# Kernel tuning notes

Measured on AMD Instinct MI355X. Metric: run time of the kernel, lower is better.

Reference implementation:

```python
import jax, jax.numpy as jnp
import numpy as np

NUM_CLUSTERS = 8
DIM_IN, DIM_HID = 1024, 256
N = 65536


def setup_inputs() -> dict:
    key = jax.random.key(0)
    ks = jax.random.split(key, 12)
    s_in = 1.0 / np.sqrt(DIM_IN)
    s_h = 1.0 / np.sqrt(DIM_HID)
    return {
        "x_path": jax.random.normal(ks[0], (1, N, DIM_IN), dtype=jnp.float32),
        "cluster_id": jax.random.randint(ks[1], (N,), 0, NUM_CLUSTERS),
        "W1": jax.random.normal(ks[2], (DIM_HID, DIM_IN), dtype=jnp.float32) * s_in,
        "b1": jax.random.normal(ks[3], (DIM_HID,), dtype=jnp.float32) * s_in,
        "Wf": jax.random.normal(ks[4], (DIM_HID, DIM_HID), dtype=jnp.float32) * s_h,
        "bf": jax.random.normal(ks[5], (DIM_HID,), dtype=jnp.float32) * s_h,
        "Wa": jax.random.normal(ks[6], (DIM_HID, DIM_HID), dtype=jnp.float32) * s_h,
        "ba": jax.random.normal(ks[7], (DIM_HID,), dtype=jnp.float32) * s_h,
        "Wb": jax.random.normal(ks[8], (DIM_HID, DIM_HID), dtype=jnp.float32) * s_h,
        "bb": jax.random.normal(ks[9], (DIM_HID,), dtype=jnp.float32) * s_h,
        "Wc": jax.random.normal(ks[10], (1, DIM_HID), dtype=jnp.float32) * s_h,
        "bc": jax.random.normal(ks[11], (1,), dtype=jnp.float32) * s_h,
    }


def reference(x_path, cluster_id, W1, b1, Wf, bf, Wa, ba, Wb, bb, Wc, bc):
    x = x_path[0]  # [N, dim_in]
    # per-instance 1x1 conv + ReLU (== linear + ReLU)
    h = jax.nn.relu(jnp.einsum('nd,hd->nh', x, W1) + b1)  # [N, dim_hid]
    # segment mean over clusters (AdaptiveAvgPool1d(1) per cluster); empty -> 0
    seg_sum = jax.ops.segment_sum(h, cluster_id, num_segments=NUM_CLUSTERS)
    counts = jax.ops.segment_sum(jnp.ones((h.shape[0],), h.dtype), cluster_id,
                                 num_segments=NUM_CLUSTERS)
    h_cluster = seg_sum / jnp.maximum(counts, 1.0)[:, None]  # [K, dim_hid]
    # attention net: Linear + ReLU (dropout is inference identity)
    h_path = jax.nn.relu(h_cluster @ Wf.T + bf)  # [K, dim_hid]
    # gated attention (CLAM Attn_Net_Gated)
    a = jnp.tanh(h_path @ Wa.T + ba)
    g = jax.nn.sigmoid(h_path @ Wb.T + bb)
    A = (a * g) @ Wc.T + bc            # [K, 1]
    A = jax.nn.softmax(A.T, axis=1)    # [1, K]
    H = A @ h_path                     # [1, dim_hid]
    return H
```

## Files before the change

kernel.cpp:

```cpp
#include <hip/hip_runtime.h>
#include <hip/hip_bf16.h>

#define NN    65536
#define KDIM  1024
#define HDIM  256
#define NC    8
#define BM    64
#define NPH   32

typedef __bf16 bf16x8 __attribute__((ext_vector_type(8)));
typedef float  f32x4  __attribute__((ext_vector_type(4)));
typedef __attribute__((address_space(1))) void GV;
typedef __attribute__((address_space(3))) void LV;

static __device__ __forceinline__ void async_cp16(const void* g, void* l) {
    __builtin_amdgcn_global_load_lds((GV*)g, (LV*)l, 16, 0, 0);
}

#define WAIT_VM6()        __builtin_amdgcn_s_waitcnt(0x0F76)
#define WAIT_VM4()        __builtin_amdgcn_s_waitcnt(0x0F74)
#define WAIT_VM6_LGKM0()  __builtin_amdgcn_s_waitcnt(0x0076)
#define SCHED_PIN()       __builtin_amdgcn_sched_barrier(0)

static __device__ __forceinline__ unsigned short f2bf_rne(float f) {
    unsigned int u = __float_as_uint(f);
    unsigned int r = u + 0x7fffu + ((u >> 16) & 1u);
    return (unsigned short)(r >> 16);
}

static __device__ __forceinline__ unsigned long long pack4bf(float4 v) {
    return (unsigned long long)f2bf_rne(v.x)
         | ((unsigned long long)f2bf_rne(v.y) << 16)
         | ((unsigned long long)f2bf_rne(v.z) << 32)
         | ((unsigned long long)f2bf_rne(v.w) << 48);
}

static __device__ __forceinline__ bf16x8 cvt8(f32x4 a, f32x4 b) {
    __hip_bfloat162 p0 = __float22bfloat162_rn(float2{a[0], a[1]});
    __hip_bfloat162 p1 = __float22bfloat162_rn(float2{a[2], a[3]});
    __hip_bfloat162 p2 = __float22bfloat162_rn(float2{b[0], b[1]});
    __hip_bfloat162 p3 = __float22bfloat162_rn(float2{b[2], b[3]});
    union { __hip_bfloat162 h[4]; bf16x8 v; } u;
    u.h[0] = p0; u.h[1] = p1; u.h[2] = p2; u.h[3] = p3;
    return u.v;
}

__global__ __launch_bounds__(256) void prep_kernel(
    const float* __restrict__ W1, unsigned short* __restrict__ W1b,
    const int* __restrict__ cid, int* __restrict__ cnt_partial)
{
    __shared__ int hcnt[NC];
    if (threadIdx.x < NC) hcnt[threadIdx.x] = 0;
    __syncthreads();

    const int gid  = blockIdx.x * 256 + threadIdx.x;
    const int lane = gid & 63;
    const int j    = (gid >> 6) & 3;
    const int wv   = (gid >> 8) & 3;
    const int kb   = gid >> 10;
    const int n    = wv * 64 + j * 16 + (lane & 15);
    const int k0   = kb * 32 + (lane >> 4) * 8;
    const float* src = W1 + (size_t)n * KDIM + k0;
    float4 v0 = *(const float4*)(src);
    float4 v1 = *(const float4*)(src + 4);
    ulonglong2 pk;
    pk.x = pack4bf(v0);
    pk.y = pack4bf(v1);
    *(ulonglong2*)(W1b + (size_t)gid * 8) = pk;

    atomicAdd(&hcnt[cid[gid]], 1);
    atomicAdd(&hcnt[cid[gid + 32768]], 1);
    __syncthreads();
    if (threadIdx.x < NC)
        cnt_partial[blockIdx.x * NC + threadIdx.x] = hcnt[threadIdx.x];
}

__global__ __launch_bounds__(256, 4) void gemm_kernel(
    const float* __restrict__ x, const int* __restrict__ cid,
    const unsigned short* __restrict__ W1b, const float* __restrict__ b1,
    float* __restrict__ partial)
{
    __shared__ __align__(16) char xs[3 * 8192];
    __shared__ float lsums[HDIM * NC];
    __shared__ int cids[BM];

    const int tid  = threadIdx.x;
    const int wave = tid >> 6;
    const int lane = tid & 63;
    const int l15  = lane & 15;
    const int q    = lane >> 4;
    const int row0 = blockIdx.x * BM;

    for (int i = tid; i < HDIM * NC; i += 256) lsums[i] = 0.0f;
    if (tid < BM) cids[tid] = cid[row0 + tid];

    const int rl = lane >> 3;
    const int cl = (lane & 7) ^ rl;
    const float* xg = x + (size_t)(row0 + wave * 16 + rl) * KDIM + cl * 4;

    const unsigned short* bg = W1b + (size_t)(wave * 256 + lane) * 8;

    const int le0 = l15 * 128 + (((2 * q + 0) ^ (l15 & 7)) * 16);
    const int le1 = l15 * 128 + (((2 * q + 1) ^ (l15 & 7)) * 16);

    f32x4 acc[4][4];
    #pragma unroll
    for (int i = 0; i < 4; ++i)
        #pragma unroll
        for (int j = 0; j < 4; ++j)
            #pragma unroll
            for (int r = 0; r < 4; ++r) acc[i][j][r] = 0.0f;

    bf16x8 bA[4], bB[4];

    #pragma unroll
    for (int h = 0; h < 2; ++h)
        async_cp16(xg + (size_t)h * 8 * KDIM, &xs[wave * 2048 + h * 1024]);
    #pragma unroll
    for (int j = 0; j < 4; ++j)
        bA[j] = *(const bf16x8*)(bg + j * 512);
    #pragma unroll
    for (int h = 0; h < 2; ++h)
        async_cp16(xg + (size_t)h * 8 * KDIM + 32, &xs[8192 + wave * 2048 + h * 1024]);
    SCHED_PIN();
    WAIT_VM6_LGKM0();
    __builtin_amdgcn_s_barrier();
    SCHED_PIN();

    #pragma unroll
    for (int kb = 0; kb < NPH; ++kb) {
        const int buf = kb % 3;
        bf16x8* curB = (kb & 1) ? bB : bA;
        bf16x8* nxtB = (kb & 1) ? bA : bB;

        if (kb + 1 < NPH) {
            #pragma unroll
            for (int j = 0; j < 4; ++j)
                nxtB[j] = *(const bf16x8*)(bg + (size_t)(kb + 1) * 8192 + j * 512);
        }
        if (kb + 2 < NPH) {
            const int b2 = (kb + 2) % 3;
            #pragma unroll
            for (int h = 0; h < 2; ++h)
                async_cp16(xg + (size_t)h * 8 * KDIM + (kb + 2) * 32,
                           &xs[b2 * 8192 + wave * 2048 + h * 1024]);
        }

        bf16x8 af[4];
        #pragma unroll
        for (int i = 0; i < 4; ++i) {
            const f32x4 v0 = *(const f32x4*)&xs[buf * 8192 + i * 2048 + le0];
            const f32x4 v1 = *(const f32x4*)&xs[buf * 8192 + i * 2048 + le1];
            af[i] = cvt8(v0, v1);
        }
        #pragma unroll
        for (int i = 0; i < 4; ++i)
            #pragma unroll
            for (int j = 0; j < 4; ++j)
                acc[i][j] = __builtin_amdgcn_mfma_f32_16x16x32_bf16(af[i], curB[j], acc[i][j], 0, 0, 0);

        if (kb < NPH - 2) {
            SCHED_PIN();
            if (kb < NPH - 2 - 1 + 1 && kb + 2 < NPH) WAIT_VM6(); else WAIT_VM4();
            __builtin_amdgcn_s_barrier();
            SCHED_PIN();
        } else if (kb == NPH - 2) {
            SCHED_PIN();
            WAIT_VM4();
            __builtin_amdgcn_s_barrier();
            SCHED_PIN();
        }
    }

    float b1v[4];
    #pragma unroll
    for (int j = 0; j < 4; ++j) b1v[j] = b1[wave * 64 + j * 16 + l15];

    #pragma unroll
    for (int i = 0; i < 4; ++i) {
        #pragma unroll
        for (int j = 0; j < 4; ++j) {
            const int col = wave * 64 + j * 16 + l15;
            #pragma unroll
            for (int r = 0; r < 4; ++r) {
                float v = fmaxf(acc[i][j][r] + b1v[j], 0.0f);
                int m = i * 16 + q * 4 + r;
                atomicAdd(&lsums[col * NC + cids[m]], v);
            }
        }
    }
    __syncthreads();
    float* dst = partial + (size_t)blockIdx.x * 2048 + tid * 8;
    *(f32x4*)dst       = *(const f32x4*)&lsums[tid * 8];
    *(f32x4*)(dst + 4) = *(const f32x4*)&lsums[tid * 8 + 4];
}

__global__ __launch_bounds__(256) void reduce_kernel(
    const float* __restrict__ partial, float* __restrict__ stage2)
{
    const int s  = blockIdx.x >> 3;
    const int og = blockIdx.x & 7;
    const int o  = og * 256 + threadIdx.x;
    const float* p = partial + (size_t)s * 128 * 2048 + o;
    float a0=0,a1=0,a2=0,a3=0,a4=0,a5=0,a6=0,a7=0;
    #pragma unroll 4
    for (int pb = 0; pb < 128; pb += 8) {
        a0 += p[(size_t)(pb+0)*2048]; a1 += p[(size_t)(pb+1)*2048];
        a2 += p[(size_t)(pb+2)*2048]; a3 += p[(size_t)(pb+3)*2048];
        a4 += p[(size_t)(pb+4)*2048]; a5 += p[(size_t)(pb+5)*2048];
        a6 += p[(size_t)(pb+6)*2048]; a7 += p[(size_t)(pb+7)*2048];
    }
    stage2[(size_t)s * 2048 + o] = ((a0+a1)+(a2+a3)) + ((a4+a5)+(a6+a7));
}

__global__ __launch_bounds__(256) void head_kernel(
    const float* __restrict__ stage2, const int* __restrict__ cnt_partial,
    const float* __restrict__ Wf, const float* __restrict__ bf1,
    const float* __restrict__ Wa, const float* __restrict__ ba,
    const float* __restrict__ Wb, const float* __restrict__ bb,
    const float* __restrict__ Wc, const float* __restrict__ bc,
    float* __restrict__ out)
{
    __shared__ float hcT[HDIM * NC];
    __shared__ float hpT[HDIM * NC];
    __shared__ float red[NC * 4];
    __shared__ int   cnt_s[256];
    __shared__ float cnt_f[NC];
    const int c = threadIdx.x;
    const int wave = c >> 6, lane = c & 63;

    {
        int k = c & 7, g = c >> 3;
        const int* cp = cnt_partial + g * 32 + k;
        cnt_s[c] = cp[0] + cp[8] + cp[16] + cp[24];
    }
    __syncthreads();
    if (c < NC) {
        int s = 0;
        #pragma unroll
        for (int g = 0; g < 32; ++g) s += cnt_s[g * 8 + c];
        cnt_f[c] = 1.0f / fmaxf((float)s, 1.0f);
    }
    __syncthreads();

    {
        float a[NC] = {0,0,0,0,0,0,0,0};
        #pragma unroll
        for (int s = 0; s < 8; ++s) {
            f32x4 u0 = *(const f32x4*)&stage2[(size_t)s * 2048 + c * 8];
            f32x4 u1 = *(const f32x4*)&stage2[(size_t)s * 2048 + c * 8 + 4];
            a[0]+=u0[0]; a[1]+=u0[1]; a[2]+=u0[2]; a[3]+=u0[3];
            a[4]+=u1[0]; a[5]+=u1[1]; a[6]+=u1[2]; a[7]+=u1[3];
        }
        #pragma unroll
        for (int k = 0; k < NC; ++k) hcT[c * NC + k] = a[k] * cnt_f[k];
    }
    __syncthreads();

    {
        float acc[NC];
        float bias = bf1[c];
        #pragma unroll
        for (int k = 0; k < NC; ++k) acc[k] = bias;
        const float4* wf4 = (const float4*)(Wf + (size_t)c * HDIM);
        for (int d4 = 0; d4 < 64; ++d4) {
            float4 w = wf4[d4];
            #pragma unroll
            for (int e = 0; e < 4; ++e) {
                float wd = (e == 0) ? w.x : (e == 1) ? w.y : (e == 2) ? w.z : w.w;
                const f32x4 h0 = *(const f32x4*)&hcT[(d4 * 4 + e) * NC];
                const f32x4 h1 = *(const f32x4*)&hcT[(d4 * 4 + e) * NC + 4];
                acc[0] += wd * h0[0]; acc[1] += wd * h0[1];
                acc[2] += wd * h0[2]; acc[3] += wd * h0[3];
                acc[4] += wd * h1[0]; acc[5] += wd * h1[1];
                acc[6] += wd * h1[2]; acc[7] += wd * h1[3];
            }
        }
        #pragma unroll
        for (int k = 0; k < NC; ++k) hpT[c * NC + k] = fmaxf(acc[k], 0.0f);
    }
    __syncthreads();

    float za[NC], zb[NC];
    {
        float biasa = ba[c], biasb = bb[c];
        #pragma unroll
        for (int k = 0; k < NC; ++k) { za[k] = biasa; zb[k] = biasb; }
        const float4* wa4 = (const float4*)(Wa + (size_t)c * HDIM);
        const float4* wb4 = (const float4*)(Wb + (size_t)c * HDIM);
        for (int d4 = 0; d4 < 64; ++d4) {
            float4 wa = wa4[d4], wb = wb4[d4];
            #pragma unroll
            for (int e = 0; e < 4; ++e) {
                float wav = (e == 0) ? wa.x : (e == 1) ? wa.y : (e == 2) ? wa.z : wa.w;
                float wbv = (e == 0) ? wb.x : (e == 1) ? wb.y : (e == 2) ? wb.z : wb.w;
                const f32x4 h0 = *(const f32x4*)&hpT[(d4 * 4 + e) * NC];
                const f32x4 h1 = *(const f32x4*)&hpT[(d4 * 4 + e) * NC + 4];
                za[0] += wav * h0[0]; za[1] += wav * h0[1]; za[2] += wav * h0[2]; za[3] += wav * h0[3];
                za[4] += wav * h1[0]; za[5] += wav * h1[1]; za[6] += wav * h1[2]; za[7] += wav * h1[3];
                zb[0] += wbv * h0[0]; zb[1] += wbv * h0[1]; zb[2] += wbv * h0[2]; zb[3] += wbv * h0[3];
                zb[4] += wbv * h1[0]; zb[5] += wbv * h1[1]; zb[6] += wbv * h1[2]; zb[7] += wbv * h1[3];
            }
        }
    }
    float wcv = Wc[c];
    float v[NC];
    #pragma unroll
    for (int k = 0; k < NC; ++k) {
        float a = tanhf(za[k]);
        float g = 1.0f / (1.0f + expf(-zb[k]));
        v[k] = a * g * wcv;
    }
    #pragma unroll
    for (int k = 0; k < NC; ++k) {
        float s = v[k];
        #pragma unroll
        for (int off = 32; off > 0; off >>= 1) s += __shfl_down(s, off, 64);
        if (lane == 0) red[k * 4 + wave] = s;
    }
    __syncthreads();
    float logit[NC], m = -1e30f;
    #pragma unroll
    for (int k = 0; k < NC; ++k) {
        logit[k] = red[k * 4] + red[k * 4 + 1] + red[k * 4 + 2] + red[k * 4 + 3] + bc[0];
        m = fmaxf(m, logit[k]);
    }
    float s = 0.0f, ex[NC];
    #pragma unroll
    for (int k = 0; k < NC; ++k) { ex[k] = expf(logit[k] - m); s += ex[k]; }
    float inv = 1.0f / s;
    float o = 0.0f;
    #pragma unroll
    for (int k = 0; k < NC; ++k) o += ex[k] * inv * hpT[c * NC + k];
    out[c] = o;
}

extern "C" void kernel_launch(void* const* d_in, const int* in_sizes, int n_in,
                              void* d_out, int out_size, void* d_ws, size_t ws_size,
                              hipStream_t stream)
{
    (void)in_sizes; (void)n_in; (void)out_size; (void)ws_size;
    const float* x   = (const float*)d_in[0];
    const int*   cid = (const int*)  d_in[1];
    const float* W1  = (const float*)d_in[2];
    const float* b1  = (const float*)d_in[3];
    const float* Wf  = (const float*)d_in[4];
    const float* bfv = (const float*)d_in[5];
    const float* Wa  = (const float*)d_in[6];
    const float* ba  = (const float*)d_in[7];
    const float* Wb  = (const float*)d_in[8];
    const float* bb  = (const float*)d_in[9];
    const float* Wc  = (const float*)d_in[10];
    const float* bc  = (const float*)d_in[11];
    float* out = (float*)d_out;

    unsigned short* W1b   = (unsigned short*)d_ws;
    int*   cnt_partial    = (int*)  ((char*)d_ws + 524288);
    float* partial        = (float*)((char*)d_ws + 528384);
    float* stage2         = (float*)((char*)d_ws + 528384 + 8388608);

    hipLaunchKernelGGL(prep_kernel,   dim3(128),     dim3(256), 0, stream, W1, W1b, cid, cnt_partial);
    hipLaunchKernelGGL(gemm_kernel,   dim3(NN / BM), dim3(256), 0, stream, x, cid, W1b, b1, partial);
    hipLaunchKernelGGL(reduce_kernel, dim3(64),      dim3(256), 0, stream, partial, stage2);
    hipLaunchKernelGGL(head_kernel,   dim3(1),       dim3(256), 0, stream,
                       stage2, cnt_partial, Wf, bfv, Wa, ba, Wb, bb, Wc, bc, out);
}
```

Before: 526.4 us.

## Use deeper K-stages with double buffering and rotated K start per block

```diff
diff --git a/kernel.cpp b/kernel.cpp
--- a/kernel.cpp
+++ b/kernel.cpp
@@ -6,7 +6,7 @@
 #define HDIM  256
 #define NC    8
 #define BM    64
-#define NPH   32
+#define NSP   8
 
 typedef __bf16 bf16x8 __attribute__((ext_vector_type(8)));
 typedef float  f32x4  __attribute__((ext_vector_type(4)));
@@ -17,10 +17,8 @@
     __builtin_amdgcn_global_load_lds((GV*)g, (LV*)l, 16, 0, 0);
 }
 
-#define WAIT_VM6()        __builtin_amdgcn_s_waitcnt(0x0F76)
-#define WAIT_VM4()        __builtin_amdgcn_s_waitcnt(0x0F74)
-#define WAIT_VM6_LGKM0()  __builtin_amdgcn_s_waitcnt(0x0076)
-#define SCHED_PIN()       __builtin_amdgcn_sched_barrier(0)
+#define WAIT_VM16()  __builtin_amdgcn_s_waitcnt(0x4F70)
+#define SCHED_PIN()  __builtin_amdgcn_sched_barrier(0)
 
 static __device__ __forceinline__ unsigned short f2bf_rne(float f) {
     unsigned int u = __float_as_uint(f);
@@ -75,14 +73,14 @@
         cnt_partial[blockIdx.x * NC + threadIdx.x] = hcnt[threadIdx.x];
 }
 
-__global__ __launch_bounds__(256, 4) void gemm_kernel(
+__global__ __launch_bounds__(256, 2) void gemm_kernel(
     const float* __restrict__ x, const int* __restrict__ cid,
     const unsigned short* __restrict__ W1b, const float* __restrict__ b1,
     float* __restrict__ partial)
 {
-    __shared__ __align__(16) char xs[3 * 8192];
-    __shared__ float lsums[HDIM * NC];
-    __shared__ int cids[BM];
+    __shared__ __align__(16) char xs[2 * 32768];
+    float* lsums = (float*)xs;
+    int*   cids  = (int*)(xs + 8192);
 
     const int tid  = threadIdx.x;
     const int wave = tid >> 6;
@@ -90,19 +88,19 @@
     const int l15  = lane & 15;
     const int q    = lane >> 4;
     const int row0 = blockIdx.x * BM;
-
-    for (int i = tid; i < HDIM * NC; i += 256) lsums[i] = 0.0f;
-    if (tid < BM) cids[tid] = cid[row0 + tid];
-
-    const int rl = lane >> 3;
-    const int cl = (lane & 7) ^ rl;
-    const float* xg = x + (size_t)(row0 + wave * 16 + rl) * KDIM + cl * 4;
+    const int rot  = blockIdx.x & 7;
+
+    int myc = 0;
+    if (tid < BM) myc = cid[row0 + tid];
+
+    const int lrow  = lane >> 5;
+    const int lslot = lane & 31;
+
+    const int le0 = l15 * 512 + (((2 * q + 0) ^ (l15 & 7)) << 4);
+    const int le1 = l15 * 512 + (((2 * q + 1) ^ (l15 & 7)) << 4);
 
     const unsigned short* bg = W1b + (size_t)(wave * 256 + lane) * 8;
 
-    const int le0 = l15 * 128 + (((2 * q + 0) ^ (l15 & 7)) * 16);
-    const int le1 = l15 * 128 + (((2 * q + 1) ^ (l15 & 7)) * 16);
-
     f32x4 acc[4][4];
     #pragma unroll
     for (int i = 0; i < 4; ++i)
@@ -111,66 +109,83 @@
             #pragma unroll
             for (int r = 0; r < 4; ++r) acc[i][j][r] = 0.0f;
 
-    bf16x8 bA[4], bB[4];
-
-    #pragma unroll
-    for (int h = 0; h < 2; ++h)
-        async_cp16(xg + (size_t)h * 8 * KDIM, &xs[wave * 2048 + h * 1024]);
-    #pragma unroll
-    for (int j = 0; j < 4; ++j)
-        bA[j] = *(const bf16x8*)(bg + j * 512);
-    #pragma unroll
-    for (int h = 0; h < 2; ++h)
-        async_cp16(xg + (size_t)h * 8 * KDIM + 32, &xs[8192 + wave * 2048 + h * 1024]);
-    SCHED_PIN();
-    WAIT_VM6_LGKM0();
-    __builtin_amdgcn_s_barrier();
-    SCHED_PIN();
-
-    #pragma unroll
-    for (int kb = 0; kb < NPH; ++kb) {
-        const int buf = kb % 3;
-        bf16x8* curB = (kb & 1) ? bB : bA;
-        bf16x8* nxtB = (kb & 1) ? bA : bB;
-
-        if (kb + 1 < NPH) {
+    bf16x8 bA[16], bB[16];
+
+    {
+        const int pp0 = rot;
+        #pragma unroll
+        for (int t = 0; t < 8; ++t) {
+            const int r7 = (2 * t + lrow) & 7;
+            const float* src = x + (size_t)(row0 + wave * 16 + 2 * t + lrow) * KDIM
+                             + pp0 * 128 + ((lslot ^ r7) << 2);
+            async_cp16(src, &xs[(wave * 8 + t) * 1024]);
+        }
+        SCHED_PIN();
+        #pragma unroll
+        for (int ks = 0; ks < 4; ++ks)
             #pragma unroll
             for (int j = 0; j < 4; ++j)
-                nxtB[j] = *(const bf16x8*)(bg + (size_t)(kb + 1) * 8192 + j * 512);
-        }
-        if (kb + 2 < NPH) {
-            const int b2 = (kb + 2) % 3;
-            #pragma unroll
-            for (int h = 0; h < 2; ++h)
-                async_cp16(xg + (size_t)h * 8 * KDIM + (kb + 2) * 32,
-                           &xs[b2 * 8192 + wave * 2048 + h * 1024]);
-        }
-
-        bf16x8 af[4];
-        #pragma unroll
-        for (int i = 0; i < 4; ++i) {
-            const f32x4 v0 = *(const f32x4*)&xs[buf * 8192 + i * 2048 + le0];
-            const f32x4 v1 = *(const f32x4*)&xs[buf * 8192 + i * 2048 + le1];
-            af[i] = cvt8(v0, v1);
-        }
-        #pragma unroll
-        for (int i = 0; i < 4; ++i)
-            #pragma unroll
-            for (int j = 0; j < 4; ++j)
-                acc[i][j] = __builtin_amdgcn_mfma_f32_16x16x32_bf16(af[i], curB[j], acc[i][j], 0, 0, 0);
-
-        if (kb < NPH - 2) {
+                bA[ks * 4 + j] = *(const bf16x8*)(bg + (size_t)(pp0 * 4 + ks) * 8192 + j * 512);
+        SCHED_PIN();
+        WAIT_VM16();
+        __builtin_amdgcn_s_barrier();
+        SCHED_PIN();
+    }
+
+    #pragma unroll
+    for (int p = 0; p < NSP; ++p) {
+        const int buf = p & 1;
+        bf16x8* curB = (p & 1) ? bB : bA;
+        bf16x8* nxtB = (p & 1) ? bA : bB;
+
+        if (p + 1 < NSP) {
+            const int pp1 = (p + 1 + rot) & 7;
+            #pragma unroll
+            for (int t = 0; t < 8; ++t) {
+                const int r7 = (2 * t + lrow) & 7;
+                const float* src = x + (size_t)(row0 + wave * 16 + 2 * t + lrow) * KDIM
+                                 + pp1 * 128 + ((lslot ^ r7) << 2);
+                async_cp16(src, &xs[(1 - buf) * 32768 + (wave * 8 + t) * 1024]);
+            }
             SCHED_PIN();
-            if (kb < NPH - 2 - 1 + 1 && kb + 2 < NPH) WAIT_VM6(); else WAIT_VM4();
+            #pragma unroll
+            for (int ks = 0; ks < 4; ++ks)
+                #pragma unroll
+                for (int j = 0; j < 4; ++j)
+                    nxtB[ks * 4 + j] = *(const bf16x8*)(bg + (size_t)(pp1 * 4 + ks) * 8192 + j * 512);
+        }
+
+        #pragma unroll
+        for (int ks = 0; ks < 4; ++ks) {
+            bf16x8 af[4];
+            #pragma unroll
+            for (int i = 0; i < 4; ++i) {
+                const f32x4 v0 = *(const f32x4*)&xs[buf * 32768 + i * 8192 + ks * 128 + le0];
+                const f32x4 v1 = *(const f32x4*)&xs[buf * 32768 + i * 8192 + ks * 128 + le1];
+                af[i] = cvt8(v0, v1);
+            }
+            #pragma unroll
+            for (int i = 0; i < 4; ++i)
+                #pragma unroll
+                for (int j = 0; j < 4; ++j)
+                    acc[i][j] = __builtin_amdgcn_mfma_f32_16x16x32_bf16(af[i], curB[ks * 4 + j], acc[i][j], 0, 0, 0);
+        }
+
+        if (p + 1 < NSP) {
+            SCHED_PIN();
+            WAIT_VM16();
             __builtin_amdgcn_s_barrier();
             SCHED_PIN();
-        } else if (kb == NPH - 2) {
-            SCHED_PIN();
-            WAIT_VM4();
-            __builtin_amdgcn_s_barrier();
-            SCHED_PIN();
-        }
-    }
+        }
+    }
+
+    {
+        const f32x4 z = {0.0f, 0.0f, 0.0f, 0.0f};
+        *(f32x4*)&lsums[tid * 8]     = z;
+        *(f32x4*)&lsums[tid * 8 + 4] = z;
+        if (tid < BM) cids[tid] = myc;
+    }
+    __syncthreads();
 
     float b1v[4];
     #pragma unroll
```

After: 500.1 us. 5.0% less time.
